# Performance work log

Measured on AMD Instinct MI355X. Metric: run time of the kernel, lower is better.

The kernel has to match this reference:

```python
import jax, jax.numpy as jnp
import numpy as np

N, E = 100000, 3200000
IN, HID, OUT = 512, 256, 64
K, ALPHA = 10, 0.1


def setup_inputs() -> dict:
    key = jax.random.key(0)
    k1, k2, k3, k4, k5, k6 = jax.random.split(key, 6)
    x = jax.random.normal(k1, (N, IN), dtype=jnp.float32)
    edge_index = jax.random.randint(k2, (2, E), 0, N, dtype=jnp.int64)
    s1 = 1.0 / np.sqrt(IN)
    s2 = 1.0 / np.sqrt(HID)
    # nn.Linear default init: U(-1/sqrt(fan_in), 1/sqrt(fan_in))
    W1 = jax.random.uniform(k3, (IN, HID), jnp.float32, -s1, s1)
    b1 = jax.random.uniform(k4, (HID,), jnp.float32, -s1, s1)
    W2 = jax.random.uniform(k5, (HID, OUT), jnp.float32, -s2, s2)
    b2 = jax.random.uniform(k6, (OUT,), jnp.float32, -s2, s2)
    return {"x": x, "edge_index": edge_index, "W1": W1, "b1": b1, "W2": W2, "b2": b2}


def reference(x, edge_index, W1, b1, W2, b2):
    # MLP (dropout is identity in eval mode)
    h = jax.nn.relu(x @ W1 + b1) @ W2 + b2  # [N, OUT]

    # gcn_norm with self-loops (PyG APPNP default, normalize=True)
    loop = jnp.arange(N, dtype=edge_index.dtype)
    src = jnp.concatenate([edge_index[0], loop])  # message sources
    dst = jnp.concatenate([edge_index[1], loop])  # aggregation targets
    deg = jax.ops.segment_sum(jnp.ones_like(dst, dtype=h.dtype), dst, num_segments=N)
    dinv = jnp.where(deg > 0, jax.lax.rsqrt(jnp.maximum(deg, 1.0)), 0.0)
    norm = (dinv[src] * dinv[dst])[:, None]  # [E+N, 1]

    x0 = h
    def step(hk, _):
        agg = jax.ops.segment_sum(norm * hk[src], dst, num_segments=N)
        return (1.0 - ALPHA) * agg + ALPHA * x0, None

    h, _ = jax.lax.scan(step, h, None, length=K)
    return h
```

## Files before the change

kernel.cpp:

```cpp
#include <hip/hip_runtime.h>
#include <hip/hip_bf16.h>

#define IN_F  512
#define HID_F 256
#define OUT_F 64

#define BSHIFT 9
#define BNODES 512
#define NBK_MAX 256
#define EBUF_CAP 18432
#define CURS 16
#define CHUNK 8192

typedef __attribute__((ext_vector_type(8))) short bf16x8;
typedef __attribute__((ext_vector_type(4))) float f32x4;

__device__ inline unsigned short f2bf(float f) {
    unsigned u = __float_as_uint(f);
    u += 0x7FFFu + ((u >> 16) & 1u);
    return (unsigned short)(u >> 16);
}
__device__ inline float bf2f(unsigned v) {
    return __uint_as_float(v << 16);
}

__device__ inline bf16x8 cvt8(f32x4 v0, f32x4 v1) {
    bf16x8 r;
    r[0] = (short)f2bf(v0[0]); r[1] = (short)f2bf(v0[1]);
    r[2] = (short)f2bf(v0[2]); r[3] = (short)f2bf(v0[3]);
    r[4] = (short)f2bf(v1[0]); r[5] = (short)f2bf(v1[1]);
    r[6] = (short)f2bf(v1[2]); r[7] = (short)f2bf(v1[3]);
    return r;
}

__device__ inline void gload_lds16(const void* g, void* l) {
    __builtin_amdgcn_global_load_lds(
        (const __attribute__((address_space(1))) void*)g,
        (__attribute__((address_space(3))) void*)l, 16, 0, 0);
}

__global__ void prep_w_kernel(const float* __restrict__ W1,
                              const float* __restrict__ W2,
                              unsigned short* __restrict__ W1T,
                              unsigned short* __restrict__ W2T)
{
    int i = blockIdx.x * 256 + threadIdx.x;
    if (i < IN_F * HID_F) {
        int k = i / HID_F, n = i % HID_F;
        W1T[n * IN_F + k] = f2bf(W1[i]);
    }
    if (i < HID_F * OUT_F) {
        int k = i / OUT_F, n = i % OUT_F;
        W2T[n * HID_F + k] = f2bf(W2[i]);
    }
}

__global__ __launch_bounds__(512, 4) void mlp_kernel(
    const float* __restrict__ x, const unsigned short* __restrict__ W1T,
    const float* __restrict__ b1, const unsigned short* __restrict__ W2T,
    const float* __restrict__ b2, const float* __restrict__ dinv,
    unsigned short* __restrict__ h0bf, unsigned short* __restrict__ g0, int N)
{
    __shared__ uint4 smem4[4096];
    char* smem = (char*)smem4;

    const int t  = threadIdx.x;
    const int w  = t >> 6;
    const int l  = t & 63;
    const int lr = l & 15;
    const int lq = l >> 4;
    const int wr = w & 3;
    const int wc = w >> 2;

    const int row0 = blockIdx.x * 128;

    f32x4 acc[2][8];
    #pragma unroll
    for (int s = 0; s < 2; ++s)
        #pragma unroll
        for (int f = 0; f < 8; ++f) acc[s][f] = (f32x4){0.f, 0.f, 0.f, 0.f};

    const int ar0 = row0 + wr * 32 + lr;
    const int ar1 = ar0 + 16;
    const bool av0 = ar0 < N, av1 = ar1 < N;
    const float* xp0 = x + (size_t)ar0 * IN_F + lq * 8;
    const float* xp1 = x + (size_t)ar1 * IN_F + lq * 8;

    auto stage = [&](int ks, int buf) {
        #pragma unroll
        for (int is = 0; is < 4; ++is) {
            int j  = is * 512 + t;
            int n  = j >> 3;
            int cs = (j & 7) ^ (n & 7);
            const unsigned short* srcp = W1T + (size_t)n * IN_F + ks * 64 + cs * 8;
            char* dstp = smem + buf * 32768 + is * 8192 + (t >> 6) * 1024;
            gload_lds16(srcp, dstp);
        }
    };

    f32x4 raw[8];
    auto xload = [&](int ks) {
        if (av0) {
            raw[0] = *(const f32x4*)(xp0 + ks * 64);
            raw[1] = *(const f32x4*)(xp0 + ks * 64 + 4);
            raw[2] = *(const f32x4*)(xp0 + ks * 64 + 32);
            raw[3] = *(const f32x4*)(xp0 + ks * 64 + 36);
        } else {
            raw[0] = raw[1] = raw[2] = raw[3] = (f32x4){0.f, 0.f, 0.f, 0.f};
        }
        if (av1) {
            raw[4] = *(const f32x4*)(xp1 + ks * 64);
            raw[5] = *(const f32x4*)(xp1 + ks * 64 + 4);
            raw[6] = *(const f32x4*)(xp1 + ks * 64 + 32);
            raw[7] = *(const f32x4*)(xp1 + ks * 64 + 36);
        } else {
            raw[4] = raw[5] = raw[6] = raw[7] = (f32x4){0.f, 0.f, 0.f, 0.f};
        }
    };

    stage(0, 0);
    xload(0);
    __syncthreads();

    #pragma unroll
    for (int ks = 0; ks < 8; ++ks) {
        bf16x8 afr[2][2];
        afr[0][0] = cvt8(raw[0], raw[1]);
        afr[0][1] = cvt8(raw[2], raw[3]);
        afr[1][0] = cvt8(raw[4], raw[5]);
        afr[1][1] = cvt8(raw[6], raw[7]);
        if (ks < 7) {
            stage(ks + 1, (ks + 1) & 1);
            xload(ks + 1);
        }
        const char* bb = smem + (ks & 1) * 32768;
        #pragma unroll
        for (int kh = 0; kh < 2; ++kh) {
            #pragma unroll
            for (int f = 0; f < 8; ++f) {
                int n = wc * 128 + f * 16 + lr;
                unsigned off = (unsigned)(n * 128 + kh * 64 + lq * 16);
                bf16x8 b = *(const bf16x8*)(bb + (off ^ ((unsigned)(n & 7) << 4)));
                acc[0][f] = __builtin_amdgcn_mfma_f32_16x16x32_bf16(afr[0][kh], b, acc[0][f], 0, 0, 0);
                acc[1][f] = __builtin_amdgcn_mfma_f32_16x16x32_bf16(afr[1][kh], b, acc[1][f], 0, 0, 0);
            }
        }
        __syncthreads();
    }

    #pragma unroll
    for (int f = 0; f < 8; ++f) {
        int c = wc * 128 + f * 16 + lr;
        float bbv = b1[c];
        #pragma unroll
        for (int sub = 0; sub < 2; ++sub) {
            #pragma unroll
            for (int j2 = 0; j2 < 4; ++j2) {
                int rr = wr * 32 + sub * 16 + lq * 4 + j2;
                float vv = acc[sub][f][j2] + bbv;
                vv = vv > 0.f ? vv : 0.f;
                unsigned off = (unsigned)(rr * 512 + c * 2);
                *(unsigned short*)(smem + (off ^ ((unsigned)(rr & 7) << 4))) = f2bf(vv);
            }
        }
    }
    __syncthreads();

    const int ct = w & 3;
    const int rh = w >> 2;
    f32x4 a2[4];
    #pragma unroll
    for (int m = 0; m < 4; ++m) a2[m] = (f32x4){0.f, 0.f, 0.f, 0.f};

    const unsigned short* w2p = W2T + (size_t)(ct * 16 + lr) * HID_F + lq * 8;

    #pragma unroll 2
    for (int ks = 0; ks < 8; ++ks) {
        bf16x8 bfrag = *(const bf16x8*)(w2p + ks * 32);
        #pragma unroll
        for (int m = 0; m < 4; ++m) {
            int rr = rh * 64 + m * 16 + lr;
            unsigned off = (unsigned)(rr * 512 + ks * 64 + lq * 16);
            bf16x8 afrag = *(const bf16x8*)(smem + (off ^ ((unsigned)(rr & 7) << 4)));
            a2[m] = __builtin_amdgcn_mfma_f32_16x16x32_bf16(afrag, bfrag, a2[m], 0, 0, 0);
        }
    }

    float bb2 = b2[ct * 16 + lr];
    #pragma unroll
    for (int m = 0; m < 4; ++m) {
        #pragma unroll
        for (int j2 = 0; j2 < 4; ++j2) {
            int rr = row0 + rh * 64 + m * 16 + lq * 4 + j2;
            if (rr < N) {
                float v = a2[m][j2] + bb2;
                int c = ct * 16 + lr;
                h0bf[(size_t)rr * OUT_F + c] = f2bf(v);
                g0[(size_t)rr * OUT_F + c]   = f2bf(dinv[rr] * v);
            }
        }
    }
}

__global__ __launch_bounds__(256) void binned_scatter_kernel(
    const int* __restrict__ src, const int* __restrict__ dst,
    int* __restrict__ bcur, unsigned* __restrict__ ebuf, int E, int nbk)
{
    __shared__ int hist[NBK_MAX];
    __shared__ int gbase[NBK_MAX];
    __shared__ int lcur[NBK_MAX];

    const int t  = threadIdx.x;
    const int bs = blockIdx.x * CHUNK;
    const int nE = min(CHUNK, E - bs);

    if (t < NBK_MAX) { hist[t] = 0; lcur[t] = 0; }
    __syncthreads();

    for (int j = t; j < nE; j += 256)
        atomicAdd(&hist[dst[bs + j] >> BSHIFT], 1);
    __syncthreads();

    for (int b = t; b < nbk; b += 256)
        gbase[b] = hist[b] ? atomicAdd(&bcur[b * CURS], hist[b]) : 0;
    __syncthreads();

    for (int j = t; j < nE; j += 256) {
        int d = dst[bs + j];
        int s = src[bs + j];
        int b = d >> BSHIFT;
        int r = atomicAdd(&lcur[b], 1);
        unsigned pos = (unsigned)(gbase[b] + r);
        if (pos < EBUF_CAP)
            ebuf[(size_t)b * EBUF_CAP + pos] =
                ((unsigned)(d & (BNODES - 1)) << 17) | (unsigned)s;
    }
}

__global__ __launch_bounds__(1024) void bucket_scan_kernel(
    const int* __restrict__ bcur, int* __restrict__ bbase,
    int* __restrict__ off, int nbk, int N, int E)
{
    __shared__ int sm[1024];
    int t = threadIdx.x;
    int v = 0;
    if (t < nbk) {
        v = bcur[t * CURS];
        if (v > EBUF_CAP) v = EBUF_CAP;
    }
    sm[t] = v;
    __syncthreads();
    for (int ofs = 1; ofs < 1024; ofs <<= 1) {
        int x = (t >= ofs) ? sm[t - ofs] : 0;
        __syncthreads();
        sm[t] += x;
        __syncthreads();
    }
    if (t < nbk) bbase[t] = sm[t] - v;
    if (t == nbk - 1) bbase[nbk] = sm[t];
    if (t == 0) off[N] = E;
}

__global__ __launch_bounds__(256) void bucket_build_kernel(
    const unsigned* __restrict__ ebuf, const int* __restrict__ bbase,
    float* __restrict__ dinv, int* __restrict__ off,
    int* __restrict__ csr, int N)
{
    __shared__ int cnt[BNODES];
    __shared__ int loc[BNODES];
    __shared__ int tsum[256];
    const int b = blockIdx.x;
    const int t = threadIdx.x;
    const int beg = bbase[b];
    const int nE  = bbase[b + 1] - beg;
    const unsigned* eb = ebuf + (size_t)b * EBUF_CAP;

    cnt[t] = 0; cnt[t + 256] = 0;
    __syncthreads();
    for (int j = t; j < nE; j += 256)
        atomicAdd(&cnt[eb[j] >> 17], 1);
    __syncthreads();

    int c0 = cnt[2 * t], c1 = cnt[2 * t + 1];
    tsum[t] = c0 + c1;
    __syncthreads();
    for (int ofs = 1; ofs < 256; ofs <<= 1) {
        int v = (t >= ofs) ? tsum[t - ofs] : 0;
        __syncthreads();
        tsum[t] += v;
        __syncthreads();
    }
    int base = (t == 0) ? 0 : tsum[t - 1];
    loc[2 * t]     = beg + base;
    loc[2 * t + 1] = beg + base + c0;
    __syncthreads();

    for (int u = t; u < BNODES; u += 256) {
        int node = b * BNODES + u;
        if (node < N) {
            dinv[node] = rsqrtf((float)(cnt[u] + 1));
            off[node]  = loc[u];
        }
    }
    __syncthreads();
    for (int j = t; j < nE; j += 256) {
        unsigned u = eb[j];
        int pos = atomicAdd(&loc[u >> 17], 1);
        csr[pos] = (int)(u & 0x1FFFFu);
    }
}

__global__ __launch_bounds__(256) void step_kernel(
    const unsigned short* __restrict__ gin,
    const unsigned short* __restrict__ h0bf,
    unsigned short* __restrict__ gout, float* __restrict__ outf,
    const int* __restrict__ off, const int* __restrict__ csr,
    const float* __restrict__ dinv, int N, int last)
{
    const int t    = threadIdx.x;
    const int wid  = (blockIdx.x * 256 + t) >> 6;
    if (wid >= N) return;
    const int lane = t & 63;
    const int q    = lane >> 4;
    const int fb   = lane & 15;

    const uint2* gin2 = (const uint2*)gin;

    float a0 = 0.f, a1 = 0.f, a2 = 0.f, a3 = 0.f;
    const int beg = __builtin_amdgcn_readfirstlane(off[wid]);
    const int end = __builtin_amdgcn_readfirstlane(off[wid + 1]);

    for (int i = beg; i < end; i += 32) {
        int idx[8];
        #pragma unroll
        for (int jj = 0; jj < 8; ++jj) {
            int e = i + jj * 4 + q;
            idx[jj] = (e < end) ? csr[e] : -1;
        }
        uint2 v[8];
        #pragma unroll
        for (int jj = 0; jj < 8; ++jj) {
            v[jj] = (idx[jj] >= 0) ? gin2[(size_t)idx[jj] * 16 + fb]
                                   : make_uint2(0u, 0u);
        }
        #pragma unroll
        for (int jj = 0; jj < 8; ++jj) {
            a0 += bf2f(v[jj].x & 0xffffu);
            a1 += bf2f(v[jj].x >> 16);
            a2 += bf2f(v[jj].y & 0xffffu);
            a3 += bf2f(v[jj].y >> 16);
        }
    }

    a0 += __shfl_xor(a0, 16); a0 += __shfl_xor(a0, 32);
    a1 += __shfl_xor(a1, 16); a1 += __shfl_xor(a1, 32);
    a2 += __shfl_xor(a2, 16); a2 += __shfl_xor(a2, 32);
    a3 += __shfl_xor(a3, 16); a3 += __shfl_xor(a3, 32);

    if (q == 0) {
        uint2 sv = gin2[(size_t)wid * 16 + fb];
        uint2 hv = ((const uint2*)h0bf)[(size_t)wid * 16 + fb];
        float dv = dinv[wid];
        float s0 = a0 + bf2f(sv.x & 0xffffu);
        float s1 = a1 + bf2f(sv.x >> 16);
        float s2 = a2 + bf2f(sv.y & 0xffffu);
        float s3 = a3 + bf2f(sv.y >> 16);
        float r0 = 0.9f * dv * s0 + 0.1f * bf2f(hv.x & 0xffffu);
        float r1 = 0.9f * dv * s1 + 0.1f * bf2f(hv.x >> 16);
        float r2 = 0.9f * dv * s2 + 0.1f * bf2f(hv.y & 0xffffu);
        float r3 = 0.9f * dv * s3 + 0.1f * bf2f(hv.y >> 16);
        if (last) {
            float4 o = make_float4(r0, r1, r2, r3);
            *(float4*)(outf + (size_t)wid * OUT_F + fb * 4) = o;
        } else {
            uint2 g;
            g.x = (unsigned)f2bf(dv * r0) | ((unsigned)f2bf(dv * r1) << 16);
            g.y = (unsigned)f2bf(dv * r2) | ((unsigned)f2bf(dv * r3) << 16);
            ((uint2*)gout)[(size_t)wid * 16 + fb] = g;
        }
    }
}

extern "C" void kernel_launch(void* const* d_in, const int* in_sizes, int n_in,
                              void* d_out, int out_size, void* d_ws, size_t ws_size,
                              hipStream_t stream)
{
    const float* x  = (const float*)d_in[0];
    const int*   ei = (const int*)d_in[1];
    const float* W1 = (const float*)d_in[2];
    const float* b1 = (const float*)d_in[3];
    const float* W2 = (const float*)d_in[4];
    const float* b2 = (const float*)d_in[5];
    float* out = (float*)d_out;

    const int N = in_sizes[0] / IN_F;
    const int E = in_sizes[1] / 2;
    const int* src = ei;
    const int* dst = ei + E;
    const int nbk = (N + BNODES - 1) >> BSHIFT;

    char* wsp = (char*)d_ws;
    auto alloc = [&](size_t bytes) -> char* {
        char* p = wsp;
        wsp += (bytes + 255) & ~(size_t)255;
        return p;
    };
    int*   off  = (int*)  alloc((size_t)(N + 1) * 4);
    float* dinv = (float*)alloc((size_t)N * 4);
    int*   csr  = (int*)  alloc((size_t)E * 4);
    unsigned* ebuf = (unsigned*)alloc((size_t)nbk * EBUF_CAP * 4);
    int*   bcur  = (int*) alloc((size_t)nbk * CURS * 4);
    int*   bbase = (int*) alloc((size_t)(nbk + 1) * 4);
    unsigned short* h0bf = (unsigned short*)alloc((size_t)N * OUT_F * 2);
    unsigned short* gA   = (unsigned short*)alloc((size_t)N * OUT_F * 2);
    unsigned short* gB   = (unsigned short*)alloc((size_t)N * OUT_F * 2);
    unsigned short* W1T  = (unsigned short*)alloc((size_t)IN_F * HID_F * 2);
    unsigned short* W2T  = (unsigned short*)alloc((size_t)HID_F * OUT_F * 2);

    hipMemsetAsync(bcur, 0, (size_t)nbk * CURS * 4, stream);

    const int gScat = (E + CHUNK - 1) / CHUNK;
    binned_scatter_kernel<<<gScat, 256, 0, stream>>>(src, dst, bcur, ebuf, E, nbk);
    bucket_scan_kernel<<<1, 1024, 0, stream>>>(bcur, bbase, off, nbk, N, E);
    bucket_build_kernel<<<nbk, 256, 0, stream>>>(ebuf, bbase, dinv, off, csr, N);

    prep_w_kernel<<<(IN_F * HID_F + 255) / 256, 256, 0, stream>>>(W1, W2, W1T, W2T);
    mlp_kernel<<<(N + 127) / 128, 512, 0, stream>>>(x, W1T, b1, W2T, b2, dinv,
                                                    h0bf, gA, N);

    const int gS = (N + 3) / 4;
    const unsigned short* gin = gA;
    unsigned short* gout = gB;
    for (int k = 0; k < 10; ++k) {
        int last = (k == 9);
        step_kernel<<<gS, 256, 0, stream>>>(gin, h0bf, gout, out, off, csr,
                                            dinv, N, last);
        const unsigned short* tmp = gin;
        gin = gout;
        gout = (unsigned short*)tmp;
    }
}
```

Before: 896.6 us.

## Split node features into four 16-column planes for cache-local propagation

The propagated feature arrays (h0 and g) move from row-major [N,64] bf16 to four planes of [N,16]. Each propagation step runs one block group per feature quarter, so each quarter's working set (about 3.2 MB) fits better in cache during the random neighbour gathers. A wave now gathers 16 edges at a time with 32-byte reads per neighbour and reduces across more lanes with shuffles. The MLP kernel also stops prefetching x into registers one k-step ahead and loads it directly per half-step. The cost is four times as many step blocks, each re-reading the CSR indices, plus smaller, less coalesced gather transactions.

```diff
diff --git a/kernel.cpp b/kernel.cpp
--- a/kernel.cpp
+++ b/kernel.cpp
@@ -98,51 +98,37 @@
         }
     };
 
-    f32x4 raw[8];
-    auto xload = [&](int ks) {
-        if (av0) {
-            raw[0] = *(const f32x4*)(xp0 + ks * 64);
-            raw[1] = *(const f32x4*)(xp0 + ks * 64 + 4);
-            raw[2] = *(const f32x4*)(xp0 + ks * 64 + 32);
-            raw[3] = *(const f32x4*)(xp0 + ks * 64 + 36);
-        } else {
-            raw[0] = raw[1] = raw[2] = raw[3] = (f32x4){0.f, 0.f, 0.f, 0.f};
-        }
-        if (av1) {
-            raw[4] = *(const f32x4*)(xp1 + ks * 64);
-            raw[5] = *(const f32x4*)(xp1 + ks * 64 + 4);
-            raw[6] = *(const f32x4*)(xp1 + ks * 64 + 32);
-            raw[7] = *(const f32x4*)(xp1 + ks * 64 + 36);
-        } else {
-            raw[4] = raw[5] = raw[6] = raw[7] = (f32x4){0.f, 0.f, 0.f, 0.f};
-        }
-    };
-
     stage(0, 0);
-    xload(0);
-    __syncthreads();
-
-    #pragma unroll
+    __syncthreads();
+
     for (int ks = 0; ks < 8; ++ks) {
-        bf16x8 afr[2][2];
-        afr[0][0] = cvt8(raw[0], raw[1]);
-        afr[0][1] = cvt8(raw[2], raw[3]);
-        afr[1][0] = cvt8(raw[4], raw[5]);
-        afr[1][1] = cvt8(raw[6], raw[7]);
-        if (ks < 7) {
-            stage(ks + 1, (ks + 1) & 1);
-            xload(ks + 1);
-        }
+        if (ks < 7) stage(ks + 1, (ks + 1) & 1);
         const char* bb = smem + (ks & 1) * 32768;
         #pragma unroll
         for (int kh = 0; kh < 2; ++kh) {
+            const int kofs = ks * 64 + kh * 32;
+            bf16x8 a0v, a1v;
+            if (av0) {
+                a0v = cvt8(*(const f32x4*)(xp0 + kofs),
+                           *(const f32x4*)(xp0 + kofs + 4));
+            } else {
+                #pragma unroll
+                for (int j = 0; j < 8; ++j) a0v[j] = 0;
+            }
+            if (av1) {
+                a1v = cvt8(*(const f32x4*)(xp1 + kofs),
+                           *(const f32x4*)(xp1 + kofs + 4));
+            } else {
+                #pragma unroll
+                for (int j = 0; j < 8; ++j) a1v[j] = 0;
+            }
             #pragma unroll
             for (int f = 0; f < 8; ++f) {
                 int n = wc * 128 + f * 16 + lr;
                 unsigned off = (unsigned)(n * 128 + kh * 64 + lq * 16);
                 bf16x8 b = *(const bf16x8*)(bb + (off ^ ((unsigned)(n & 7) << 4)));
-                acc[0][f] = __builtin_amdgcn_mfma_f32_16x16x32_bf16(afr[0][kh], b, acc[0][f], 0, 0, 0);
-                acc[1][f] = __builtin_amdgcn_mfma_f32_16x16x32_bf16(afr[1][kh], b, acc[1][f], 0, 0, 0);
+                acc[0][f] = __builtin_amdgcn_mfma_f32_16x16x32_bf16(a0v, b, acc[0][f], 0, 0, 0);
+                acc[1][f] = __builtin_amdgcn_mfma_f32_16x16x32_bf16(a1v, b, acc[1][f], 0, 0, 0);
             }
         }
         __syncthreads();
@@ -194,9 +180,9 @@
             int rr = row0 + rh * 64 + m * 16 + lq * 4 + j2;
             if (rr < N) {
                 float v = a2[m][j2] + bb2;
-                int c = ct * 16 + lr;
-                h0bf[(size_t)rr * OUT_F + c] = f2bf(v);
-                g0[(size_t)rr * OUT_F + c]   = f2bf(dinv[rr] * v);
+                size_t qi = ((size_t)ct * N + rr) * 16 + lr;
+                h0bf[qi] = f2bf(v);
+                g0[qi]   = f2bf(dinv[rr] * v);
             }
         }
     }
@@ -315,51 +301,49 @@
     const unsigned short* __restrict__ h0bf,
     unsigned short* __restrict__ gout, float* __restrict__ outf,
     const int* __restrict__ off, const int* __restrict__ csr,
-    const float* __restrict__ dinv, int N, int last)
-{
-    const int t    = threadIdx.x;
-    const int wid  = (blockIdx.x * 256 + t) >> 6;
+    const float* __restrict__ dinv, int N, int ngrp, int last)
+{
+    const int bid = blockIdx.x;
+    const int q   = bid / ngrp;
+    const int grp = bid - q * ngrp;
+    const int t   = threadIdx.x;
+    const int wid = grp * 4 + (t >> 6);
     if (wid >= N) return;
     const int lane = t & 63;
-    const int q    = lane >> 4;
-    const int fb   = lane & 15;
-
-    const uint2* gin2 = (const uint2*)gin;
+    const int es   = lane >> 2;
+    const int fb   = lane & 3;
+
+    const uint2* gq = (const uint2*)gin + (size_t)q * N * 4;
 
     float a0 = 0.f, a1 = 0.f, a2 = 0.f, a3 = 0.f;
     const int beg = __builtin_amdgcn_readfirstlane(off[wid]);
     const int end = __builtin_amdgcn_readfirstlane(off[wid + 1]);
 
     for (int i = beg; i < end; i += 32) {
-        int idx[8];
-        #pragma unroll
-        for (int jj = 0; jj < 8; ++jj) {
-            int e = i + jj * 4 + q;
-            idx[jj] = (e < end) ? csr[e] : -1;
-        }
-        uint2 v[8];
-        #pragma unroll
-        for (int jj = 0; jj < 8; ++jj) {
-            v[jj] = (idx[jj] >= 0) ? gin2[(size_t)idx[jj] * 16 + fb]
-                                   : make_uint2(0u, 0u);
-        }
-        #pragma unroll
-        for (int jj = 0; jj < 8; ++jj) {
-            a0 += bf2f(v[jj].x & 0xffffu);
-            a1 += bf2f(v[jj].x >> 16);
-            a2 += bf2f(v[jj].y & 0xffffu);
-            a3 += bf2f(v[jj].y >> 16);
-        }
-    }
-
+        int e0 = i + es;
+        int e1 = i + 16 + es;
+        int i0 = (e0 < end) ? csr[e0] : -1;
+        int i1 = (e1 < end) ? csr[e1] : -1;
+        uint2 v0 = (i0 >= 0) ? gq[(size_t)i0 * 4 + fb] : make_uint2(0u, 0u);
+        uint2 v1 = (i1 >= 0) ? gq[(size_t)i1 * 4 + fb] : make_uint2(0u, 0u);
+        a0 += bf2f(v0.x & 0xffffu) + bf2f(v1.x & 0xffffu);
+        a1 += bf2f(v0.x >> 16)     + bf2f(v1.x >> 16);
+        a2 += bf2f(v0.y & 0xffffu) + bf2f(v1.y & 0xffffu);
+        a3 += bf2f(v0.y >> 16)     + bf2f(v1.y >> 16);
+    }
+
+    a0 += __shfl_xor(a0, 4); a0 += __shfl_xor(a0, 8);
     a0 += __shfl_xor(a0, 16); a0 += __shfl_xor(a0, 32);
+    a1 += __shfl_xor(a1, 4); a1 += __shfl_xor(a1, 8);
     a1 += __shfl_xor(a1, 16); a1 += __shfl_xor(a1, 32);
+    a2 += __shfl_xor(a2, 4); a2 += __shfl_xor(a2, 8);
     a2 += __shfl_xor(a2, 16); a2 += __shfl_xor(a2, 32);
+    a3 += __shfl_xor(a3, 4); a3 += __shfl_xor(a3, 8);
     a3 += __shfl_xor(a3, 16); a3 += __shfl_xor(a3, 32);
 
-    if (q == 0) {
-        uint2 sv = gin2[(size_t)wid * 16 + fb];
-        uint2 hv = ((const uint2*)h0bf)[(size_t)wid * 16 + fb];
+    if (es == 0) {
+        uint2 sv = gq[(size_t)wid * 4 + fb];
+        uint2 hv = ((const uint2*)h0bf)[(size_t)q * N * 4 + (size_t)wid * 4 + fb];
         float dv = dinv[wid];
         float s0 = a0 + bf2f(sv.x & 0xffffu);
         float s1 = a1 + bf2f(sv.x >> 16);
@@ -371,12 +355,12 @@
         float r3 = 0.9f * dv * s3 + 0.1f * bf2f(hv.y >> 16);
         if (last) {
             float4 o = make_float4(r0, r1, r2, r3);
-            *(float4*)(outf + (size_t)wid * OUT_F + fb * 4) = o;
+            *(float4*)(outf + (size_t)wid * OUT_F + q * 16 + fb * 4) = o;
         } else {
             uint2 g;
             g.x = (unsigned)f2bf(dv * r0) | ((unsigned)f2bf(dv * r1) << 16);
             g.y = (unsigned)f2bf(dv * r2) | ((unsigned)f2bf(dv * r3) << 16);
-            ((uint2*)gout)[(size_t)wid * 16 + fb] = g;
+            ((uint2*)gout)[(size_t)q * N * 4 + (size_t)wid * 4 + fb] = g;
         }
     }
 }
@@ -428,13 +412,14 @@
     mlp_kernel<<<(N + 127) / 128, 512, 0, stream>>>(x, W1T, b1, W2T, b2, dinv,
                                                     h0bf, gA, N);
 
-    const int gS = (N + 3) / 4;
+    const int ngrp = (N + 3) / 4;
+    const int gS   = 4 * ngrp;
     const unsigned short* gin = gA;
     unsigned short* gout = gB;
     for (int k = 0; k < 10; ++k) {
         int last = (k == 9);
         step_kernel<<<gS, 256, 0, stream>>>(gin, h0bf, gout, out, off, csr,
-                                            dinv, N, last);
+                                            dinv, N, ngrp, last);
         const unsigned short* tmp = gin;
         gin = gout;
         gout = (unsigned short*)tmp;
```

After: 1.596 ms. +78.0%, slower.
